# Kernel optimization log

Measured on AMD Instinct MI355X. Metric: run time of the kernel, lower is better.

The kernel has to match this reference:

```python
import jax, jax.numpy as jnp
import numpy as np

B, S, L, Q = 128, 200, 50, 20   # batch, story sentences, sentence len, query len
V, D, K = 50000, 128, 3          # vocab, embed dim, n_hops


def _pe(J, d):
    # position encoding l_kj = (1 - j/J) - (k/d)(1 - 2j/J), 1-indexed
    j = jnp.arange(1, J + 1, dtype=jnp.float32)[:, None]
    k = jnp.arange(1, d + 1, dtype=jnp.float32)[None, :]
    return 1.0 - j / J - (k / d) * (1.0 - 2.0 * j / J)  # (J, d)


def setup_inputs() -> dict:
    key = jax.random.key(0)
    ks = jax.random.split(key, 5)
    story = jax.random.randint(ks[0], (B, S, L), 0, V)
    query = jax.random.randint(ks[1], (B, Q), 0, V)
    # K+1 embedding tables (adjacent weight sharing: A^{k+1} = C^k), sigma=0.1, padding row 0 zeroed
    embs = (jax.random.normal(ks[2], (K + 1, V, D)) * 0.1).at[:, 0, :].set(0.0)
    TA = jax.random.normal(ks[3], (K, S, D)) * 0.1
    TC = jax.random.normal(ks[4], (K, S, D)) * 0.1
    return {"story": story, "query": query, "embs": embs, "TA": TA, "TC": TC}


def reference(story, query, embs, TA, TC):
    d = embs.shape[-1]
    pe_s = _pe(story.shape[-1], d)   # (L, D)
    pe_q = _pe(query.shape[-1], d)   # (Q, D)
    n_hops = TA.shape[0]

    # query embedding with PE: (B, Q, D) * (Q, D) -> sum over Q -> (B, D)
    u = (jnp.take(embs[0], query, axis=0) * pe_q).sum(axis=1)

    for hop in range(n_hops):
        # gather + PE multiply + sum over words + temporal encoding: (B, S, D)
        m = (jnp.take(embs[hop], story, axis=0) * pe_s).sum(axis=2) + TA[hop]
        c = (jnp.take(embs[hop + 1], story, axis=0) * pe_s).sum(axis=2) + TC[hop]
        # attention over memory slots
        p = jax.nn.softmax(jnp.einsum('bsd,bd->bs', m, u), axis=-1)  # (B, S)
        o = jnp.einsum('bs,bsd->bd', p, c)                            # (B, D)
        u = u + o

    # final projection W = embeddings[n_hops].weight -> logits (B, V)
    return u @ embs[n_hops].T
```

## Files before the change

### kernel.cpp

```cpp
#include <hip/hip_runtime.h>

#define B 128
#define S 200
#define LW 50
#define Q 20
#define V 50000
#define D 128
#define NH 3
#define VD (V * D)
#define BSD (B * S * D)
#define BS (B * S)

typedef __bf16 bf16x8 __attribute__((ext_vector_type(8)));
typedef float f32x4 __attribute__((ext_vector_type(4)));
typedef unsigned int u32x4 __attribute__((ext_vector_type(4)));

__device__ __forceinline__ unsigned int f2bf_rne(float f) {
  union { float f; unsigned int u; } c; c.f = f;
  return (c.u + 0x7FFFu + ((c.u >> 16) & 1u)) >> 16;
}
__device__ __forceinline__ unsigned int pack2(float a, float b) {
  return f2bf_rne(a) | (f2bf_rne(b) << 16);
}
__device__ __forceinline__ float bf_lo(unsigned int q) {
  union { unsigned int u; float f; } c; c.u = q << 16; return c.f;
}
__device__ __forceinline__ float bf_hi(unsigned int q) {
  union { unsigned int u; float f; } c; c.u = q & 0xFFFF0000u; return c.f;
}

__global__ __launch_bounds__(256) void k_repack(
    const float* __restrict__ embs, unsigned int* __restrict__ ESM) {
  int v = blockIdx.x * 4 + (threadIdx.x >> 6);
  int l = threadIdx.x & 63;
  int s = l >> 4, c = l & 15;
#pragma unroll
  for (int k = 0; k < 4; ++k) {
    const float2 e = *(const float2*)(embs + (size_t)k * VD + (size_t)v * D + 2 * l);
    ESM[((size_t)(k * 4 + s) * V + v) * 16 + c] = pack2(e.x, e.y);
  }
}

__global__ __launch_bounds__(256) void k_story16(
    const int* __restrict__ story, unsigned short* __restrict__ story16) {
  int i = blockIdx.x * 256 + threadIdx.x;
  int4 v = ((const int4*)story)[i];
  ushort4 o;
  o.x = (unsigned short)v.x; o.y = (unsigned short)v.y;
  o.z = (unsigned short)v.z; o.w = (unsigned short)v.w;
  ((ushort4*)story16)[i] = o;
}

__global__ __launch_bounds__(256) void k_gather_slice(
    const unsigned short* __restrict__ story16,
    const u32x4* __restrict__ ESM4, unsigned int* __restrict__ Gp, int phase) {
  __shared__ __align__(16) unsigned short sidx[4][800];
  int unit = blockIdx.x & 7;
  int k = 2 * phase + (unit >> 2);
  int s = unit & 3;
  int widx = blockIdx.x >> 3;
  int w = threadIdx.x >> 6;
  int l = threadIdx.x & 63;
  int g = l >> 2;
  int q = l & 3;
  const u32x4* src4 = ESM4 + (size_t)(k * 4 + s) * V * 4;
  int d0 = s * 32 + 8 * q;
  float kd[8];
#pragma unroll
  for (int i = 0; i < 8; ++i) kd[i] = (float)(d0 + i + 1) * (1.0f / D);

  for (int iter = 0; iter < 2; ++iter) {
    int sent16 = widx * 128 + w * 32 + iter * 16;
    const u32x4* st4 = (const u32x4*)(story16 + sent16 * LW);
    u32x4* dst4 = (u32x4*)sidx[w];
#pragma unroll
    for (int m = 0; m < 2; ++m) {
      int e = l + m * 64;
      if (e < 100) dst4[e] = __builtin_nontemporal_load(st4 + e);
    }
    const unsigned short* wrow = sidx[w] + g * LW;
    float SA[8] = {0.f, 0.f, 0.f, 0.f, 0.f, 0.f, 0.f, 0.f};
    float SB[8] = {0.f, 0.f, 0.f, 0.f, 0.f, 0.f, 0.f, 0.f};
#pragma unroll 10
    for (int j = 0; j < LW; ++j) {
      int idx = (int)wrow[j];
      u32x4 qv = src4[(size_t)idx * 4 + q];
      float jj = (float)(j + 1) * (1.0f / LW);
      float al = 1.0f - jj;
      float bl = 2.0f * jj - 1.0f;
      float ee[8];
      ee[0] = bf_lo(qv.x); ee[1] = bf_hi(qv.x);
      ee[2] = bf_lo(qv.y); ee[3] = bf_hi(qv.y);
      ee[4] = bf_lo(qv.z); ee[5] = bf_hi(qv.z);
      ee[6] = bf_lo(qv.w); ee[7] = bf_hi(qv.w);
#pragma unroll
      for (int i = 0; i < 8; ++i) { SA[i] += ee[i] * al; SB[i] += ee[i] * bl; }
    }
    int sent = sent16 + g;
    u32x4 og;
    og.x = pack2(SA[0] + kd[0] * SB[0], SA[1] + kd[1] * SB[1]);
    og.y = pack2(SA[2] + kd[2] * SB[2], SA[3] + kd[3] * SB[3]);
    og.z = pack2(SA[4] + kd[4] * SB[4], SA[5] + kd[5] * SB[5]);
    og.w = pack2(SA[6] + kd[6] * SB[6], SA[7] + kd[7] * SB[7]);
    __builtin_nontemporal_store(
        og, (u32x4*)(Gp + ((size_t)k * BS + sent) * 64 + s * 16) + q);
  }
}

__global__ __launch_bounds__(256) void k_hops(
    const unsigned int* __restrict__ G, const int* __restrict__ query,
    const float* __restrict__ emb0, const float* __restrict__ TA,
    const float* __restrict__ TC, unsigned int* __restrict__ ubf) {
  __shared__ float su[D];
  __shared__ float sp[S];
  __shared__ float sred[2];
  __shared__ float4 oacc[8][32];
  int b = blockIdx.x;
  int t = threadIdx.x;
  if (t < D) {
    float kd = (float)(t + 1) * (1.0f / D);
    float acc = 0.f;
    for (int q = 0; q < Q; ++q) {
      int idx = query[b * Q + q];
      float jj = (float)(q + 1) * (1.0f / Q);
      float pe = 1.0f - jj - kd * (1.0f - 2.0f * jj);
      acc += emb0[(size_t)idx * D + t] * pe;
    }
    su[t] = acc;
  }
  __syncthreads();
  for (int hop = 0; hop < NH; ++hop) {
    const unsigned int* Gm = G + ((size_t)hop * BS + (size_t)b * S) * 64;
    const unsigned int* Gc = G + ((size_t)(hop + 1) * BS + (size_t)b * S) * 64;
    const float* ta = TA + hop * S * D;
    const float* tc = TC + hop * S * D;
    if (t < S) {
      float sc = 0.f;
#pragma unroll
      for (int s4 = 0; s4 < 4; ++s4)
#pragma unroll
        for (int i = 0; i < 8; ++i) {
          uint2 g2 = *(const uint2*)(Gm + (size_t)t * 64 + s4 * 16 + 2 * i);
          int d0 = s4 * 32 + 4 * i;
          float4 t4 = *(const float4*)(ta + (size_t)t * D + d0);
          sc += (bf_lo(g2.x) + t4.x) * su[d0 + 0];
          sc += (bf_hi(g2.x) + t4.y) * su[d0 + 1];
          sc += (bf_lo(g2.y) + t4.z) * su[d0 + 2];
          sc += (bf_hi(g2.y) + t4.w) * su[d0 + 3];
        }
      sp[t] = sc;
    }
    __syncthreads();
    if (t < 64) {
      float mx = -1e30f;
      for (int s = t; s < S; s += 64) mx = fmaxf(mx, sp[s]);
#pragma unroll
      for (int off = 1; off < 64; off <<= 1) mx = fmaxf(mx, __shfl_xor(mx, off));
      float sum = 0.f;
      for (int s = t; s < S; s += 64) sum += expf(sp[s] - mx);
#pragma unroll
      for (int off = 1; off < 64; off <<= 1) sum += __shfl_xor(sum, off);
      if (t == 0) { sred[0] = mx; sred[1] = sum; }
    }
    __syncthreads();
    float mx = sred[0];
    float inv = 1.0f / sred[1];
    if (t < S) sp[t] = expf(sp[t] - mx) * inv;
    __syncthreads();
    {
      int g = t >> 5, c = t & 31;
      int d0 = (c >> 3) * 32 + (c & 7) * 4;
      float4 o4 = {0.f, 0.f, 0.f, 0.f};
      for (int s = g; s < S; s += 8) {
        float p = sp[s];
        uint2 g2 = *(const uint2*)(Gc + (size_t)s * 64 + 2 * c);
        float4 t4 = *(const float4*)(tc + (size_t)s * D + d0);
        o4.x += p * (bf_lo(g2.x) + t4.x);
        o4.y += p * (bf_hi(g2.x) + t4.y);
        o4.z += p * (bf_lo(g2.y) + t4.z);
        o4.w += p * (bf_hi(g2.y) + t4.w);
      }
      oacc[g][c] = o4;
    }
    __syncthreads();
    if (t < 32) {
      int d0 = (t >> 3) * 32 + (t & 7) * 4;
      float4 o = oacc[0][t];
#pragma unroll
      for (int g = 1; g < 8; ++g) {
        float4 x = oacc[g][t];
        o.x += x.x; o.y += x.y; o.z += x.z; o.w += x.w;
      }
      su[d0 + 0] += o.x;
      su[d0 + 1] += o.y;
      su[d0 + 2] += o.z;
      su[d0 + 3] += o.w;
    }
    __syncthreads();
  }
  if (t < 64) ubf[b * 64 + t] = pack2(su[2 * t], su[2 * t + 1]);
}

__global__ __launch_bounds__(256) void k_logits_mfma(
    const uint4* __restrict__ ubf,
    const uint4* __restrict__ esm,
    float* __restrict__ out) {
  int wid = threadIdx.x >> 6;
  int l = threadIdx.x & 63;
  int lr = l & 15;
  int lk = l >> 4;
  int vbase = blockIdx.x * 128 + wid * 32;
  uint4 bfrag[2][4];
#pragma unroll
  for (int vs = 0; vs < 2; ++vs) {
    int v = vbase + vs * 16 + lr;
    if (v >= V) v = V - 1;
#pragma unroll
    for (int kk = 0; kk < 4; ++kk)
      bfrag[vs][kk] = esm[((size_t)(12 + kk) * V + v) * 4 + lk];
  }
  f32x4 acc[2][8];
#pragma unroll
  for (int vs = 0; vs < 2; ++vs)
#pragma unroll
    for (int m = 0; m < 8; ++m) {
      f32x4 z = {0.f, 0.f, 0.f, 0.f};
      acc[vs][m] = z;
    }
#pragma unroll
  for (int m = 0; m < 8; ++m) {
    uint4 afrag[4];
#pragma unroll
    for (int kk = 0; kk < 4; ++kk)
      afrag[kk] = ubf[(m * 16 + lr) * 16 + kk * 4 + lk];
#pragma unroll
    for (int vs = 0; vs < 2; ++vs)
#pragma unroll
      for (int kk = 0; kk < 4; ++kk)
        acc[vs][m] = __builtin_amdgcn_mfma_f32_16x16x32_bf16(
            __builtin_bit_cast(bf16x8, afrag[kk]),
            __builtin_bit_cast(bf16x8, bfrag[vs][kk]), acc[vs][m], 0, 0, 0);
  }
#pragma unroll
  for (int vs = 0; vs < 2; ++vs) {
    int v = vbase + vs * 16 + lr;
    if (v < V) {
#pragma unroll
      for (int m = 0; m < 8; ++m)
#pragma unroll
        for (int r = 0; r < 4; ++r)
          out[(size_t)(m * 16 + lk * 4 + r) * V + v] = acc[vs][m][r];
    }
  }
}

__global__ __launch_bounds__(128) void k_gather_query(
    const int* __restrict__ query, const float* __restrict__ embs,
    float* __restrict__ u) {
  int b = blockIdx.x;
  int d = threadIdx.x;
  float kd = (float)(d + 1) / (float)D;
  float acc = 0.f;
  for (int q = 0; q < Q; ++q) {
    int idx = query[b * Q + q];
    float jj = (float)(q + 1) / (float)Q;
    float pe = 1.0f - jj - kd * (1.0f - 2.0f * jj);
    acc += embs[(size_t)idx * D + d] * pe;
  }
  u[b * D + d] = acc;
}

__global__ __launch_bounds__(128) void k_gather_story(
    const int* __restrict__ story, const float* __restrict__ embs,
    float* __restrict__ G) {
  int bs = blockIdx.x;
  int d = threadIdx.x;
  const int* w = story + bs * LW;
  float kd = (float)(d + 1) / (float)D;
  float a0 = 0.f, a1 = 0.f, a2 = 0.f, a3 = 0.f;
  for (int l = 0; l < LW; ++l) {
    int idx = w[l];
    float jj = (float)(l + 1) / (float)LW;
    float pe = 1.0f - jj - kd * (1.0f - 2.0f * jj);
    size_t base = (size_t)idx * D + d;
    a0 += embs[base] * pe;
    a1 += embs[base + (size_t)VD] * pe;
    a2 += embs[base + (size_t)(2 * VD)] * pe;
    a3 += embs[base + (size_t)(3 * VD)] * pe;
  }
  size_t o = (size_t)bs * D + d;
  G[o] = a0;
  G[o + (size_t)BSD] = a1;
  G[o + (size_t)(2 * BSD)] = a2;
  G[o + (size_t)(3 * BSD)] = a3;
}

__global__ __launch_bounds__(256) void k_hops_f32(
    const float* __restrict__ G, const float* __restrict__ TA,
    const float* __restrict__ TC, float* __restrict__ u) {
  __shared__ float su[D];
  __shared__ float sp[S];
  __shared__ float sred[2];
  int b = blockIdx.x;
  int t = threadIdx.x;
  if (t < D) su[t] = u[b * D + t];
  __syncthreads();
  for (int hop = 0; hop < NH; ++hop) {
    const float* Gm = G + (size_t)hop * BSD + (size_t)b * S * D;
    const float* Gc = G + (size_t)(hop + 1) * BSD + (size_t)b * S * D;
    const float* ta = TA + hop * S * D;
    const float* tc = TC + hop * S * D;
    if (t < S) {
      float sc = 0.f;
      for (int d = 0; d < D; ++d) sc += (Gm[t * D + d] + ta[t * D + d]) * su[d];
      sp[t] = sc;
    }
    __syncthreads();
    if (t < 64) {
      float mx = -1e30f;
      for (int s = t; s < S; s += 64) mx = fmaxf(mx, sp[s]);
#pragma unroll
      for (int off = 1; off < 64; off <<= 1) mx = fmaxf(mx, __shfl_xor(mx, off));
      float sum = 0.f;
      for (int s = t; s < S; s += 64) sum += expf(sp[s] - mx);
#pragma unroll
      for (int off = 1; off < 64; off <<= 1) sum += __shfl_xor(sum, off);
      if (t == 0) { sred[0] = mx; sred[1] = sum; }
    }
    __syncthreads();
    float mx = sred[0];
    float inv = 1.0f / sred[1];
    if (t < S) sp[t] = expf(sp[t] - mx) * inv;
    __syncthreads();
    if (t < D) {
      float o = 0.f;
      for (int s = 0; s < S; ++s) o += sp[s] * (Gc[s * D + t] + tc[s * D + t]);
      su[t] += o;
    }
    __syncthreads();
  }
  if (t < D) u[b * D + t] = su[t];
}

__global__ __launch_bounds__(256) void k_logits_f32(
    const float* __restrict__ u, const float* __restrict__ e3,
    float* __restrict__ out) {
  __shared__ float sE[64][129];
  __shared__ float sU[64][129];
  int v0 = blockIdx.x * 64;
  int b0 = blockIdx.y * 64;
  int t = threadIdx.x;
  for (int i = 0; i < 32; ++i) {
    int lin = i * 256 + t;
    int r = lin >> 7, c = lin & 127;
    int v = v0 + r;
    sE[r][c] = (v < V) ? e3[(size_t)v * D + c] : 0.f;
    sU[r][c] = u[(b0 + r) * D + c];
  }
  __syncthreads();
  int tv = (t & 15) * 4;
  int tb = (t >> 4) * 4;
  float acc[4][4] = {};
  for (int d = 0; d < D; ++d) {
    float ev[4], ub[4];
#pragma unroll
    for (int i = 0; i < 4; ++i) ev[i] = sE[tv + i][d];
#pragma unroll
    for (int j = 0; j < 4; ++j) ub[j] = sU[tb + j][d];
#pragma unroll
    for (int j = 0; j < 4; ++j)
#pragma unroll
      for (int i = 0; i < 4; ++i) acc[j][i] += ub[j] * ev[i];
  }
  for (int j = 0; j < 4; ++j)
    for (int i = 0; i < 4; ++i) {
      int v = v0 + tv + i;
      if (v < V) out[(size_t)(b0 + tb + j) * V + v] = acc[j][i];
    }
}

extern "C" void kernel_launch(void* const* d_in, const int* in_sizes, int n_in,
                              void* d_out, int out_size, void* d_ws,
                              size_t ws_size, hipStream_t stream) {
  (void)in_sizes; (void)n_in; (void)out_size;
  const int* story = (const int*)d_in[0];
  const int* query = (const int*)d_in[1];
  const float* embs = (const float*)d_in[2];
  const float* TA = (const float*)d_in[3];
  const float* TC = (const float*)d_in[4];
  float* out = (float*)d_out;

  const size_t esm_bytes = (size_t)16 * V * 16 * 4;
  const size_t g_bytes = (size_t)4 * BS * 64 * 4;
  const size_t ub_bytes = (size_t)B * 64 * 4;
  const size_t s16_bytes = (size_t)BS * LW * 2;

  if (ws_size >= esm_bytes + g_bytes + ub_bytes + s16_bytes) {
    char* p = (char*)d_ws;
    unsigned int* ESM = (unsigned int*)p;      p += esm_bytes;
    unsigned int* Gp = (unsigned int*)p;       p += g_bytes;
    unsigned int* ubf = (unsigned int*)p;      p += ub_bytes;
    unsigned short* story16 = (unsigned short*)p;

    k_repack<<<V / 4, 256, 0, stream>>>(embs, ESM);
    k_story16<<<BS * LW / 4 / 256, 256, 0, stream>>>(story, story16);
    k_gather_slice<<<1600, 256, 0, stream>>>(story16, (const u32x4*)ESM, Gp, 0);
    k_gather_slice<<<1600, 256, 0, stream>>>(story16, (const u32x4*)ESM, Gp, 1);
    k_hops<<<B, 256, 0, stream>>>(Gp, query, embs, TA, TC, ubf);
    k_logits_mfma<<<(V + 127) / 128, 256, 0, stream>>>(
        (const uint4*)ubf, (const uint4*)ESM, out);
  } else {
    float* G = (float*)d_ws;
    float* u = G + 4 * (size_t)BSD;
    k_gather_query<<<B, D, 0, stream>>>(query, embs, u);
    k_gather_story<<<B * S, D, 0, stream>>>(story, embs, G);
    k_hops_f32<<<B, 256, 0, stream>>>(G, TA, TC, u);
    k_logits_f32<<<dim3((V + 63) / 64, B / 64), 256, 0, stream>>>(
        u, embs + 3 * (size_t)VD, out);
  }
}
```

Before: 208.5 us.

## Widen hops kernel to 1024 threads, pack TA/TC to bf16, halve gather work per block

```diff
diff --git a/kernel.cpp b/kernel.cpp
--- a/kernel.cpp
+++ b/kernel.cpp
@@ -49,6 +49,19 @@
   o.x = (unsigned short)v.x; o.y = (unsigned short)v.y;
   o.z = (unsigned short)v.z; o.w = (unsigned short)v.w;
   ((ushort4*)story16)[i] = o;
+}
+
+__global__ __launch_bounds__(256) void k_packT(
+    const float* __restrict__ TA, const float* __restrict__ TC,
+    unsigned int* __restrict__ TAp, unsigned int* __restrict__ TCp) {
+  int idx = blockIdx.x * 256 + threadIdx.x;
+  int row = idx >> 6;
+  int u = idx & 63;
+  int d0 = 32 * (u >> 4) + 2 * (u & 15);
+  const float2 a = *(const float2*)(TA + (size_t)row * D + d0);
+  const float2 c = *(const float2*)(TC + (size_t)row * D + d0);
+  TAp[idx] = pack2(a.x, a.y);
+  TCp[idx] = pack2(c.x, c.y);
 }
 
 __global__ __launch_bounds__(256) void k_gather_slice(
@@ -69,52 +82,50 @@
 #pragma unroll
   for (int i = 0; i < 8; ++i) kd[i] = (float)(d0 + i + 1) * (1.0f / D);
 
-  for (int iter = 0; iter < 2; ++iter) {
-    int sent16 = widx * 128 + w * 32 + iter * 16;
-    const u32x4* st4 = (const u32x4*)(story16 + sent16 * LW);
-    u32x4* dst4 = (u32x4*)sidx[w];
-#pragma unroll
-    for (int m = 0; m < 2; ++m) {
-      int e = l + m * 64;
-      if (e < 100) dst4[e] = __builtin_nontemporal_load(st4 + e);
-    }
-    const unsigned short* wrow = sidx[w] + g * LW;
-    float SA[8] = {0.f, 0.f, 0.f, 0.f, 0.f, 0.f, 0.f, 0.f};
-    float SB[8] = {0.f, 0.f, 0.f, 0.f, 0.f, 0.f, 0.f, 0.f};
+  int sent16 = widx * 64 + w * 16;
+  const u32x4* st4 = (const u32x4*)(story16 + sent16 * LW);
+  u32x4* dst4 = (u32x4*)sidx[w];
+#pragma unroll
+  for (int m = 0; m < 2; ++m) {
+    int e = l + m * 64;
+    if (e < 100) dst4[e] = __builtin_nontemporal_load(st4 + e);
+  }
+  const unsigned short* wrow = sidx[w] + g * LW;
+  float SA[8] = {0.f, 0.f, 0.f, 0.f, 0.f, 0.f, 0.f, 0.f};
+  float SB[8] = {0.f, 0.f, 0.f, 0.f, 0.f, 0.f, 0.f, 0.f};
 #pragma unroll 10
-    for (int j = 0; j < LW; ++j) {
-      int idx = (int)wrow[j];
-      u32x4 qv = src4[(size_t)idx * 4 + q];
-      float jj = (float)(j + 1) * (1.0f / LW);
-      float al = 1.0f - jj;
-      float bl = 2.0f * jj - 1.0f;
-      float ee[8];
-      ee[0] = bf_lo(qv.x); ee[1] = bf_hi(qv.x);
-      ee[2] = bf_lo(qv.y); ee[3] = bf_hi(qv.y);
-      ee[4] = bf_lo(qv.z); ee[5] = bf_hi(qv.z);
-      ee[6] = bf_lo(qv.w); ee[7] = bf_hi(qv.w);
-#pragma unroll
-      for (int i = 0; i < 8; ++i) { SA[i] += ee[i] * al; SB[i] += ee[i] * bl; }
-    }
-    int sent = sent16 + g;
-    u32x4 og;
-    og.x = pack2(SA[0] + kd[0] * SB[0], SA[1] + kd[1] * SB[1]);
-    og.y = pack2(SA[2] + kd[2] * SB[2], SA[3] + kd[3] * SB[3]);
-    og.z = pack2(SA[4] + kd[4] * SB[4], SA[5] + kd[5] * SB[5]);
-    og.w = pack2(SA[6] + kd[6] * SB[6], SA[7] + kd[7] * SB[7]);
-    __builtin_nontemporal_store(
-        og, (u32x4*)(Gp + ((size_t)k * BS + sent) * 64 + s * 16) + q);
-  }
-}
-
-__global__ __launch_bounds__(256) void k_hops(
-    const unsigned int* __restrict__ G, const int* __restrict__ query,
-    const float* __restrict__ emb0, const float* __restrict__ TA,
-    const float* __restrict__ TC, unsigned int* __restrict__ ubf) {
+  for (int j = 0; j < LW; ++j) {
+    int idx = (int)wrow[j];
+    u32x4 qv = src4[(size_t)idx * 4 + q];
+    float jj = (float)(j + 1) * (1.0f / LW);
+    float al = 1.0f - jj;
+    float bl = 2.0f * jj - 1.0f;
+    float ee[8];
+    ee[0] = bf_lo(qv.x); ee[1] = bf_hi(qv.x);
+    ee[2] = bf_lo(qv.y); ee[3] = bf_hi(qv.y);
+    ee[4] = bf_lo(qv.z); ee[5] = bf_hi(qv.z);
+    ee[6] = bf_lo(qv.w); ee[7] = bf_hi(qv.w);
+#pragma unroll
+    for (int i = 0; i < 8; ++i) { SA[i] += ee[i] * al; SB[i] += ee[i] * bl; }
+  }
+  int sent = sent16 + g;
+  u32x4 og;
+  og.x = pack2(SA[0] + kd[0] * SB[0], SA[1] + kd[1] * SB[1]);
+  og.y = pack2(SA[2] + kd[2] * SB[2], SA[3] + kd[3] * SB[3]);
+  og.z = pack2(SA[4] + kd[4] * SB[4], SA[5] + kd[5] * SB[5]);
+  og.w = pack2(SA[6] + kd[6] * SB[6], SA[7] + kd[7] * SB[7]);
+  __builtin_nontemporal_store(
+      og, (u32x4*)(Gp + ((size_t)k * BS + sent) * 64 + s * 16) + q);
+}
+
+__global__ __launch_bounds__(1024) void k_hops(
+    const unsigned int* __restrict__ G, const unsigned int* __restrict__ TAp,
+    const unsigned int* __restrict__ TCp, const int* __restrict__ query,
+    const float* __restrict__ emb0, unsigned int* __restrict__ ubf) {
   __shared__ float su[D];
   __shared__ float sp[S];
   __shared__ float sred[2];
-  __shared__ float4 oacc[8][32];
+  __shared__ float4 oacc[32][32];
   int b = blockIdx.x;
   int t = threadIdx.x;
   if (t < D) {
@@ -132,23 +143,26 @@
   for (int hop = 0; hop < NH; ++hop) {
     const unsigned int* Gm = G + ((size_t)hop * BS + (size_t)b * S) * 64;
     const unsigned int* Gc = G + ((size_t)(hop + 1) * BS + (size_t)b * S) * 64;
-    const float* ta = TA + hop * S * D;
-    const float* tc = TC + hop * S * D;
-    if (t < S) {
+    const unsigned int* ta = TAp + (size_t)hop * S * 64;
+    const unsigned int* tc = TCp + (size_t)hop * S * 64;
+    if (t < 4 * S) {
+      int sl = t >> 2, p = t & 3;
+      const uint2* gr = (const uint2*)(Gm + (size_t)sl * 64 + p * 16);
+      const uint2* tr = (const uint2*)(ta + (size_t)sl * 64 + p * 16);
       float sc = 0.f;
 #pragma unroll
-      for (int s4 = 0; s4 < 4; ++s4)
-#pragma unroll
-        for (int i = 0; i < 8; ++i) {
-          uint2 g2 = *(const uint2*)(Gm + (size_t)t * 64 + s4 * 16 + 2 * i);
-          int d0 = s4 * 32 + 4 * i;
-          float4 t4 = *(const float4*)(ta + (size_t)t * D + d0);
-          sc += (bf_lo(g2.x) + t4.x) * su[d0 + 0];
-          sc += (bf_hi(g2.x) + t4.y) * su[d0 + 1];
-          sc += (bf_lo(g2.y) + t4.z) * su[d0 + 2];
-          sc += (bf_hi(g2.y) + t4.w) * su[d0 + 3];
-        }
-      sp[t] = sc;
+      for (int i = 0; i < 8; ++i) {
+        uint2 g2 = gr[i];
+        uint2 t2 = tr[i];
+        int dd = p * 32 + 4 * i;
+        sc += (bf_lo(g2.x) + bf_lo(t2.x)) * su[dd + 0];
+        sc += (bf_hi(g2.x) + bf_hi(t2.x)) * su[dd + 1];
+        sc += (bf_lo(g2.y) + bf_lo(t2.y)) * su[dd + 2];
+        sc += (bf_hi(g2.y) + bf_hi(t2.y)) * su[dd + 3];
+      }
+      sc += __shfl_xor(sc, 1);
+      sc += __shfl_xor(sc, 2);
+      if (p == 0) sp[sl] = sc;
     }
     __syncthreads();
     if (t < 64) {
@@ -169,16 +183,15 @@
     __syncthreads();
     {
       int g = t >> 5, c = t & 31;
-      int d0 = (c >> 3) * 32 + (c & 7) * 4;
       float4 o4 = {0.f, 0.f, 0.f, 0.f};
-      for (int s = g; s < S; s += 8) {
+      for (int s = g; s < S; s += 32) {
         float p = sp[s];
         uint2 g2 = *(const uint2*)(Gc + (size_t)s * 64 + 2 * c);
-        float4 t4 = *(const float4*)(tc + (size_t)s * D + d0);
-        o4.x += p * (bf_lo(g2.x) + t4.x);
-        o4.y += p * (bf_hi(g2.x) + t4.y);
-        o4.z += p * (bf_lo(g2.y) + t4.z);
-        o4.w += p * (bf_hi(g2.y) + t4.w);
+        uint2 t2 = *(const uint2*)(tc + (size_t)s * 64 + 2 * c);
+        o4.x += p * (bf_lo(g2.x) + bf_lo(t2.x));
+        o4.y += p * (bf_hi(g2.x) + bf_hi(t2.x));
+        o4.z += p * (bf_lo(g2.y) + bf_lo(t2.y));
+        o4.w += p * (bf_hi(g2.y) + bf_hi(t2.y));
       }
       oacc[g][c] = o4;
     }
@@ -187,7 +200,7 @@
       int d0 = (t >> 3) * 32 + (t & 7) * 4;
       float4 o = oacc[0][t];
 #pragma unroll
-      for (int g = 1; g < 8; ++g) {
+      for (int g = 1; g < 32; ++g) {
         float4 x = oacc[g][t];
         o.x += x.x; o.y += x.y; o.z += x.z; o.w += x.w;
       }
@@ -394,19 +407,23 @@
   const size_t g_bytes = (size_t)4 * BS * 64 * 4;
   const size_t ub_bytes = (size_t)B * 64 * 4;
   const size_t s16_bytes = (size_t)BS * LW * 2;
-
-  if (ws_size >= esm_bytes + g_bytes + ub_bytes + s16_bytes) {
+  const size_t tp_bytes = (size_t)NH * S * 64 * 4;
+
+  if (ws_size >= esm_bytes + g_bytes + ub_bytes + s16_bytes + 2 * tp_bytes) {
     char* p = (char*)d_ws;
     unsigned int* ESM = (unsigned int*)p;      p += esm_bytes;
     unsigned int* Gp = (unsigned int*)p;       p += g_bytes;
     unsigned int* ubf = (unsigned int*)p;      p += ub_bytes;
-    unsigned short* story16 = (unsigned short*)p;
+    unsigned short* story16 = (unsigned short*)p;  p += s16_bytes;
+    unsigned int* TAp = (unsigned int*)p;      p += tp_bytes;
+    unsigned int* TCp = (unsigned int*)p;
 
     k_repack<<<V / 4, 256, 0, stream>>>(embs, ESM);
     k_story16<<<BS * LW / 4 / 256, 256, 0, stream>>>(story, story16);
-    k_gather_slice<<<1600, 256, 0, stream>>>(story16, (const u32x4*)ESM, Gp, 0);
-    k_gather_slice<<<1600, 256, 0, stream>>>(story16, (const u32x4*)ESM, Gp, 1);
-    k_hops<<<B, 256, 0, stream>>>(Gp, query, embs, TA, TC, ubf);
+    k_packT<<<NH * S * 64 / 256, 256, 0, stream>>>(TA, TC, TAp, TCp);
+    k_gather_slice<<<3200, 256, 0, stream>>>(story16, (const u32x4*)ESM, Gp, 0);
+    k_gather_slice<<<3200, 256, 0, stream>>>(story16, (const u32x4*)ESM, Gp, 1);
+    k_hops<<<B, 1024, 0, stream>>>(Gp, TAp, TCp, query, embs, ubf);
     k_logits_mfma<<<(V + 127) / 128, 256, 0, stream>>>(
         (const uint4*)ubf, (const uint4*)ESM, out);
   } else {
```

Result: faster. 171.0 us (-18.0%).
